# Kernel optimization log

Hardware: AMD Instinct MI355X
Metric: run time of the kernel (lower is better)

The kernel has to match this reference:

```python
import jax, jax.numpy as jnp
import numpy as np

B, S, D, H, L = 4, 2048, 256, 4, 2
DK = D // H
V, T = 32000, 1000


def setup_inputs() -> dict:
    key = jax.random.key(0)
    ks = jax.random.split(key, 20)
    sc = 0.02
    event_emb = jax.random.normal(ks[0], (V, D), jnp.float32) * sc
    event_emb = event_emb.at[0].set(0.0)  # padding_idx=0
    time_emb = jax.random.normal(ks[1], (T, D), jnp.float32) * sc
    inp = {
        "x": jax.random.randint(ks[2], (B, S), 0, V, jnp.int32),
        "time_deltas": jax.random.randint(ks[3], (B, S), 0, T, jnp.int32),
        "mask": jax.random.randint(ks[4], (B, S), 0, 2, jnp.int32),
        "event_emb": event_emb,
        "time_emb": time_emb,
        "Wq": jax.random.normal(ks[5], (L, D, D), jnp.float32) * sc,
        "bq": jnp.zeros((L, D), jnp.float32),
        "Wk": jax.random.normal(ks[6], (L, D, D), jnp.float32) * sc,
        "bk": jnp.zeros((L, D), jnp.float32),
        "Wv": jax.random.normal(ks[7], (L, D, D), jnp.float32) * sc,
        "bv": jnp.zeros((L, D), jnp.float32),
        "time_proj": jax.random.normal(ks[8], (L, T, H), jnp.float32) * sc,
        "Wo": jax.random.normal(ks[9], (L, D, D), jnp.float32) * sc,
        "bo": jnp.zeros((L, D), jnp.float32),
        "ln_g": jnp.ones((L, D), jnp.float32),
        "ln_b": jnp.zeros((L, D), jnp.float32),
        "Wc1": jax.random.normal(ks[10], (D, D // 2), jnp.float32) * sc,
        "bc1": jnp.zeros((D // 2,), jnp.float32),
        "Wc2": jax.random.normal(ks[11], (D // 2, 1), jnp.float32) * sc,
        "bc2": jnp.zeros((1,), jnp.float32),
    }
    return inp


def _layernorm(h, g, b, eps=1e-5):
    mu = jnp.mean(h, -1, keepdims=True)
    var = jnp.mean(jnp.square(h - mu), -1, keepdims=True)
    return (h - mu) * jax.lax.rsqrt(var + eps) * g + b


def _attn(h, t_bins, mask, Wq, bq, Wk, bk, Wv, bv, tp, Wo, bo):
    b, s, d = h.shape
    q = (h @ Wq + bq).reshape(b, s, H, DK)
    k = (h @ Wk + bk).reshape(b, s, H, DK)
    v = (h @ Wv + bv).reshape(b, s, H, DK)
    scores = jnp.einsum("bqhd,bkhd->bhqk", q, k) / np.sqrt(DK).astype(np.float32)
    time_bias = tp[t_bins]  # [b,s,H] -> bias per key position
    scores = scores + jnp.transpose(time_bias, (0, 2, 1))[:, :, None, :]
    scores = jnp.where(mask[:, None, None, :] == 0, -1e9, scores)
    attn = jax.nn.softmax(scores, axis=-1)
    ctx = jnp.einsum("bhqk,bkhd->bqhd", attn, v).reshape(b, s, d)
    return ctx @ Wo + bo


def reference(x, time_deltas, mask, event_emb, time_emb, Wq, bq, Wk, bk, Wv, bv,
              time_proj, Wo, bo, ln_g, ln_b, Wc1, bc1, Wc2, bc2):
    t_bins = jnp.clip(time_deltas, 0, T - 1)
    h = event_emb[x] + time_emb[t_bins]
    for l in range(L):
        h = _attn(h, t_bins, mask, Wq[l], bq[l], Wk[l], bk[l], Wv[l], bv[l],
                  time_proj[l], Wo[l], bo[l])
        h = _layernorm(h, ln_g[l], ln_b[l])
    last = h[:, -1, :]
    hid = jax.nn.relu(last @ Wc1 + bc1)
    return jax.nn.sigmoid(hid @ Wc2 + bc2)
```

## Files before the change

### kernel.cpp

```cpp
#include <hip/hip_runtime.h>
#include <math.h>

namespace {

constexpr int NB = 4, NS = 2048, ND = 256, NH = 4, NDK = 64, NL = 2, NT = 1000;
constexpr float L2E = 1.44269504089f;
constexpr float QSCALE = 0.125f * L2E;

typedef short bfx8 __attribute__((ext_vector_type(8)));
typedef float f32x4 __attribute__((ext_vector_type(4)));

static __device__ __forceinline__ short f2bf(float f) {
  union { float f; unsigned u; } v; v.f = f;
  unsigned u = v.u;
  unsigned r = (u + 0x7fffu + ((u >> 16) & 1u)) >> 16;
  return (short)r;
}
static __device__ __forceinline__ float exp2_hw(float x) {
  float r;
  asm("v_exp_f32 %0, %1" : "=v"(r) : "v"(x));
  return r;
}
static __device__ __forceinline__ unsigned cvt_pk_bf16(float lo, float hi) {
  unsigned d;
  asm("v_cvt_pk_bf16_f32 %0, %1, %2" : "=v"(d) : "v"(lo), "v"(hi));
  return d;
}

__global__ __launch_bounds__(256) void k_packw(const float* __restrict__ Wq,
                                               const float* __restrict__ Wk,
                                               const float* __restrict__ Wv,
                                               const float* __restrict__ Wo,
                                               short* __restrict__ wqkvT,
                                               short* __restrict__ woT) {
  __shared__ float t[64][65];
  int z = blockIdx.z, l = z >> 2, mat = z & 3;
  const float* src;
  short* dst;
  float scale = 1.f;
  if (mat == 0)      { src = Wq + (size_t)l * 65536; dst = wqkvT + (size_t)l * 768 * 256; scale = QSCALE; }
  else if (mat == 1) { src = Wk + (size_t)l * 65536; dst = wqkvT + (size_t)l * 768 * 256 + 256 * 256; }
  else if (mat == 2) { src = Wv + (size_t)l * 65536; dst = wqkvT + (size_t)l * 768 * 256 + 512 * 256; }
  else               { src = Wo + (size_t)l * 65536; dst = woT + (size_t)l * 65536; }
  int k0 = blockIdx.x * 64, n0 = blockIdx.y * 64;
  int c = threadIdx.x & 63, r4 = threadIdx.x >> 6;
  #pragma unroll
  for (int rr = 0; rr < 64; rr += 4) t[rr + r4][c] = src[(size_t)(k0 + rr + r4) * 256 + n0 + c];
  __syncthreads();
  #pragma unroll
  for (int rr = 0; rr < 64; rr += 4) {
    int n = rr + r4;
    dst[(size_t)(n0 + n) * 256 + k0 + c] = f2bf(t[c][n] * scale);
  }
}

__global__ __launch_bounds__(768) void k_packb(const float* __restrict__ bq,
                                               const float* __restrict__ bk,
                                               const float* __restrict__ bv,
                                               float* __restrict__ bqkv) {
  int l = blockIdx.x, c = threadIdx.x;
  float v;
  if (c < 256) v = bq[l * 256 + c] * QSCALE;
  else if (c < 512) v = bk[l * 256 + c - 256];
  else v = bv[l * 256 + c - 512];
  bqkv[l * 768 + c] = v;
}

__global__ __launch_bounds__(256) void k_embed(const int* __restrict__ x,
                                               const int* __restrict__ td,
                                               const float* __restrict__ ee,
                                               const float* __restrict__ te,
                                               float* __restrict__ h,
                                               short* __restrict__ hb) {
  int lane = threadIdx.x & 63, r4 = threadIdx.x >> 6;
  int row = blockIdx.x * 4 + r4;
  int xi = x[row];
  int tb = td[row];
  tb = tb < 0 ? 0 : (tb >= NT ? NT - 1 : tb);
  float4 e = ((const float4*)&ee[(size_t)xi * ND])[lane];
  float4 tv = ((const float4*)&te[(size_t)tb * ND])[lane];
  float4 v;
  v.x = e.x + tv.x; v.y = e.y + tv.y; v.z = e.z + tv.z; v.w = e.w + tv.w;
  ((float4*)&h[(size_t)row * ND])[lane] = v;
  short4 ob; ob.x = f2bf(v.x); ob.y = f2bf(v.y); ob.z = f2bf(v.z); ob.w = f2bf(v.w);
  ((short4*)&hb[(size_t)row * ND])[lane] = ob;
}

template <int OUT_BF16>
__global__ __launch_bounds__(256) void k_gemm(const short* __restrict__ A,
                                              const short* __restrict__ BT,
                                              const float* __restrict__ bias,
                                              void* __restrict__ C, int ldc,
                                              int mb_mul, int mb_add, int n_base) {
  constexpr int LP = 76;
  __shared__ short at[64][LP];
  __shared__ short bt[128][LP];
  int tid = threadIdx.x;
  int w = tid >> 6, lane = tid & 63, ln15 = lane & 15, g = lane >> 4;
  int m0 = (blockIdx.x * mb_mul + mb_add) * 64;
  int n0 = n_base + blockIdx.y * 128;
  int srow = tid >> 2, scol = (tid & 3) * 16;
  int brow = tid >> 1, bcol = (tid & 1) * 32;

  f32x4 acc[8];
  #pragma unroll
  for (int nt = 0; nt < 8; ++nt) acc[nt] = (f32x4){0.f, 0.f, 0.f, 0.f};

  bfx8 a0, a1, b0, b1, b2, b3;
  auto LOAD = [&](int kk0) {
    const short* as = &A[(size_t)(m0 + srow) * 256 + kk0 + scol];
    a0 = *(const bfx8*)as; a1 = *(const bfx8*)(as + 8);
    const short* bs = &BT[(size_t)(n0 + brow) * 256 + kk0 + bcol];
    b0 = *(const bfx8*)bs; b1 = *(const bfx8*)(bs + 8);
    b2 = *(const bfx8*)(bs + 16); b3 = *(const bfx8*)(bs + 24);
  };
  LOAD(0);
  for (int kk0 = 0; kk0 < 256; kk0 += 64) {
    __syncthreads();
    *(bfx8*)&at[srow][scol] = a0; *(bfx8*)&at[srow][scol + 8] = a1;
    *(bfx8*)&bt[brow][bcol] = b0; *(bfx8*)&bt[brow][bcol + 8] = b1;
    *(bfx8*)&bt[brow][bcol + 16] = b2; *(bfx8*)&bt[brow][bcol + 24] = b3;
    if (kk0 + 64 < 256) LOAD(kk0 + 64);
    __syncthreads();
    #pragma unroll
    for (int ks = 0; ks < 2; ++ks) {
      bfx8 af = *(const bfx8*)&at[w * 16 + ln15][ks * 32 + g * 8];
      #pragma unroll
      for (int nt = 0; nt < 8; ++nt) {
        bfx8 bf = *(const bfx8*)&bt[nt * 16 + ln15][ks * 32 + g * 8];
        acc[nt] = __builtin_amdgcn_mfma_f32_16x16x32_bf16(af, bf, acc[nt], 0, 0, 0);
      }
    }
  }

  #pragma unroll
  for (int nt = 0; nt < 8; ++nt) {
    int col = n0 + nt * 16 + ln15;
    float bb = bias[col];
    #pragma unroll
    for (int r = 0; r < 4; ++r) {
      int row = m0 + w * 16 + g * 4 + r;
      float val = acc[nt][r] + bb;
      if (OUT_BF16) ((short*)C)[(size_t)row * ldc + col] = f2bf(val);
      else          ((float*)C)[(size_t)row * ldc + col] = val;
    }
  }
}

__global__ __launch_bounds__(512, 4) void k_attn(const short* __restrict__ qkv,
                                                 const int* __restrict__ td,
                                                 const int* __restrict__ mask,
                                                 const float* __restrict__ tp,
                                                 short* __restrict__ ctx,
                                                 float* __restrict__ partO,
                                                 float* __restrict__ partML,
                                                 int q_base, int nchunk) {
  constexpr int LPK = 100;
  constexpr int LPV = 76;
  __shared__ short kt[2][64][LPK];
  __shared__ short vt[2][80][LPV];

  int tid = threadIdx.x;
  int w = tid >> 6, lane = tid & 63, ln15 = lane & 15, g = lane >> 4;
  int half = w >> 2, wsub = w & 3;
  int t = tid & 255;
  int b = blockIdx.z, hh = blockIdx.y;
  int qtile = blockIdx.x / nchunk;
  int chunk = blockIdx.x - qtile * nchunk;
  int niter = NS / (128 * nchunk);
  int kbase = chunk * (NS / nchunk);
  int q0 = q_base + qtile * 64;
  int qw0 = q0 + wsub * 16;

  for (int idx = tid; idx < 2 * 64 * 35; idx += 512) {
    int h2 = idx / (64 * 35), rem = idx % (64 * 35);
    kt[h2][rem / 35][65 + rem % 35] = 0;
  }
  for (int idx = tid; idx < 2 * 16 * LPV; idx += 512) {
    int h2 = idx / (16 * LPV), rem = idx % (16 * LPV), j = rem / LPV, c = rem % LPV;
    vt[h2][64 + j][c] = (j == 0 && c < 64) ? (short)0x3F80 : (short)0;
  }

  bfx8 aq[3];
  #pragma unroll
  for (int ks = 0; ks < 2; ++ks)
    aq[ks] = *(const bfx8*)&qkv[(size_t)(b * NS + qw0 + ln15) * 768 + hh * NDK + ks * 32 + g * 8];
  {
    bfx8 z = (bfx8){0, 0, 0, 0, 0, 0, 0, 0};
    if (g == 0) z[0] = (short)0x3F80;
    aq[2] = z;
  }

  f32x4 o[5];
  #pragma unroll
  for (int dt = 0; dt < 5; ++dt) o[dt] = (f32x4){0.f, 0.f, 0.f, 0.f};
  float m = -1e30f;

  int srow = t >> 2, scg = (t & 3) * 16;
  bool needB = (t & 3) == 0;
  int vlane = t & 63, vw4 = (t >> 6) & 3;
  int pks = vlane >> 5, ptt = (vlane >> 4) & 1, pgg = (vlane >> 2) & 3, prr = vlane & 3;
  int vcol = pks * 32 + pgg * 8 + ptt * 4 + prr;

  auto loadset = [&](int it, bfx8& KR0, bfx8& KR1, bfx8& VR0, bfx8& VR1, float& BR) {
    int k0 = kbase + (half * niter + it) * 64;
    const short* ksrc = &qkv[(size_t)(b * NS + k0 + srow) * 768 + 256 + hh * NDK + scg];
    KR0 = *(const bfx8*)ksrc; KR1 = *(const bfx8*)(ksrc + 8);
    const short* vsrc = &qkv[(size_t)(b * NS + k0 + vlane) * 768 + 512 + hh * NDK + vw4 * 16];
    VR0 = *(const bfx8*)vsrc; VR1 = *(const bfx8*)(vsrc + 8);
    if (needB) {
      int key = k0 + srow;
      int tb = td[b * NS + key];
      tb = tb < 0 ? 0 : (tb >= NT ? NT - 1 : tb);
      BR = mask[b * NS + key] ? tp[tb * NH + hh] * L2E : -1e9f;
    }
  };

  auto compute = [&]() {
    f32x4 c[4];
    #pragma unroll
    for (int nt = 0; nt < 4; ++nt) {
      c[nt] = (f32x4){0.f, 0.f, 0.f, 0.f};
      #pragma unroll
      for (int ks = 0; ks < 3; ++ks) {
        bfx8 kf = *(const bfx8*)&kt[half][nt * 16 + ln15][ks * 32 + g * 8];
        c[nt] = __builtin_amdgcn_mfma_f32_16x16x32_bf16(kf, aq[ks], c[nt], 0, 0, 0);
      }
    }
    float rm = c[0][0];
    #pragma unroll
    for (int nt = 0; nt < 4; ++nt)
      #pragma unroll
      for (int r = 0; r < 4; ++r) rm = fmaxf(rm, c[nt][r]);
    rm = fmaxf(rm, __shfl_xor(rm, 16, 64));
    rm = fmaxf(rm, __shfl_xor(rm, 32, 64));
    if (__any(rm > m + 10.f)) {
      float nm = fmaxf(m, rm);
      float scl = exp2_hw(m - nm);
      m = nm;
      #pragma unroll
      for (int dt = 0; dt < 5; ++dt)
        #pragma unroll
        for (int r = 0; r < 4; ++r) o[dt][r] *= scl;
    }
    unsigned pb[2][4];
    #pragma unroll
    for (int nt = 0; nt < 4; ++nt) {
      float e0 = exp2_hw(c[nt][0] - m), e1 = exp2_hw(c[nt][1] - m);
      float e2 = exp2_hw(c[nt][2] - m), e3 = exp2_hw(c[nt][3] - m);
      pb[nt >> 1][(nt & 1) * 2]     = cvt_pk_bf16(e0, e1);
      pb[nt >> 1][(nt & 1) * 2 + 1] = cvt_pk_bf16(e2, e3);
    }
    #pragma unroll
    for (int ks = 0; ks < 2; ++ks) {
      union { unsigned u[4]; bfx8 v; } pf;
      pf.u[0] = pb[ks][0]; pf.u[1] = pb[ks][1]; pf.u[2] = pb[ks][2]; pf.u[3] = pb[ks][3];
      #pragma unroll
      for (int dt = 0; dt < 5; ++dt) {
        bfx8 vf = *(const bfx8*)&vt[half][dt * 16 + ln15][ks * 32 + g * 8];
        o[dt] = __builtin_amdgcn_mfma_f32_16x16x32_bf16(vf, pf.v, o[dt], 0, 0, 0);
      }
    }
  };

  auto body = [&](bfx8& KR0, bfx8& KR1, bfx8& VR0, bfx8& VR1, float& BR,
                  int pf_it, bool do_pf) {
    __syncthreads();
    *(bfx8*)&kt[half][srow][scg] = KR0;
    *(bfx8*)&kt[half][srow][scg + 8] = KR1;
    if (needB) kt[half][srow][64] = f2bf(BR);
    #pragma unroll
    for (int i = 0; i < 8; ++i) {
      vt[half][vw4 * 16 + i][vcol] = VR0[i];
      vt[half][vw4 * 16 + 8 + i][vcol] = VR1[i];
    }
    if (do_pf) loadset(pf_it, KR0, KR1, VR0, VR1, BR);
    __syncthreads();
    compute();
  };

  bfx8 krA0, krA1, vrA0, vrA1; float brA = 0.f;
  bfx8 krB0, krB1, vrB0, vrB1; float brB = 0.f;
  loadset(0, krA0, krA1, vrA0, vrA1, brA);
  if (niter > 1) loadset(1, krB0, krB1, vrB0, vrB1, brB);

  for (int it = 0; it < niter; it += 2) {
    body(krA0, krA1, vrA0, vrA1, brA, it + 2, it + 2 < niter);
    if (it + 1 < niter)
      body(krB0, krB1, vrB0, vrB1, brB, it + 3, it + 3 < niter);
  }

  float* shO = (float*)&kt[0][0][0];
  float* shML = (float*)&vt[0][0][0];
  __syncthreads();
  int q = wsub * 16 + ln15;
  if (half == 1) {
    #pragma unroll
    for (int dt = 0; dt < 4; ++dt) {
      float4 st; st.x = o[dt][0]; st.y = o[dt][1]; st.z = o[dt][2]; st.w = o[dt][3];
      *(float4*)&shO[q * 68 + dt * 16 + g * 4] = st;
    }
    if (g == 0) { shML[q * 2] = m; shML[q * 2 + 1] = o[4][0]; }
  }
  __syncthreads();
  if (half == 0) {
    float l = __shfl(o[4][0], ln15, 64);
    float m2 = shML[q * 2], l2 = shML[q * 2 + 1];
    float M = fmaxf(m, m2);
    float fa = exp2_hw(m - M), fb = exp2_hw(m2 - M);
    if (nchunk == 1) {
      float inv = 1.f / (l * fa + l2 * fb);
      fa *= inv; fb *= inv;
      #pragma unroll
      for (int dt = 0; dt < 4; ++dt) {
        float4 sh = *(const float4*)&shO[q * 68 + dt * 16 + g * 4];
        float v0 = o[dt][0] * fa + sh.x * fb;
        float v1 = o[dt][1] * fa + sh.y * fb;
        float v2 = o[dt][2] * fa + sh.z * fb;
        float v3 = o[dt][3] * fa + sh.w * fb;
        int2 pk; pk.x = (int)cvt_pk_bf16(v0, v1); pk.y = (int)cvt_pk_bf16(v2, v3);
        *(int2*)&ctx[(size_t)(b * NS + q0 + q) * ND + hh * NDK + dt * 16 + g * 4] = pk;
      }
    } else {
      float L = l * fa + l2 * fb;
      size_t pidx = (size_t)(chunk * NB + b) * NH + hh;
      #pragma unroll
      for (int dt = 0; dt < 4; ++dt) {
        float4 sh = *(const float4*)&shO[q * 68 + dt * 16 + g * 4];
        float4 st;
        st.x = o[dt][0] * fa + sh.x * fb;
        st.y = o[dt][1] * fa + sh.y * fb;
        st.z = o[dt][2] * fa + sh.z * fb;
        st.w = o[dt][3] * fa + sh.w * fb;
        *(float4*)&partO[pidx * 4096 + q * 64 + dt * 16 + g * 4] = st;
      }
      if (g == 0) { partML[pidx * 128 + q * 2] = M; partML[pidx * 128 + q * 2 + 1] = L; }
    }
  }
}

__global__ __launch_bounds__(256) void k_amerge(const float* __restrict__ partO,
                                                const float* __restrict__ partML,
                                                short* __restrict__ ctx,
                                                int q_base, int nchunk) {
  int b = blockIdx.x, hh = blockIdx.y;
  int q = threadIdx.x >> 2, d0 = (threadIdx.x & 3) * 16;
  float M = -1e30f;
  for (int c = 0; c < nchunk; ++c)
    M = fmaxf(M, partML[((size_t)(c * NB + b) * NH + hh) * 128 + q * 2]);
  float L = 0.f;
  float acc[16];
  #pragma unroll
  for (int i = 0; i < 16; ++i) acc[i] = 0.f;
  for (int c = 0; c < nchunk; ++c) {
    size_t pidx = (size_t)(c * NB + b) * NH + hh;
    float mc = partML[pidx * 128 + q * 2];
    float lc = partML[pidx * 128 + q * 2 + 1];
    float s = exp2_hw(mc - M);
    L += lc * s;
    const float4* op = (const float4*)&partO[pidx * 4096 + q * 64 + d0];
    #pragma unroll
    for (int i = 0; i < 4; ++i) {
      float4 v = op[i];
      acc[i * 4]     += v.x * s;
      acc[i * 4 + 1] += v.y * s;
      acc[i * 4 + 2] += v.z * s;
      acc[i * 4 + 3] += v.w * s;
    }
  }
  float inv = 1.f / L;
  short res[16];
  #pragma unroll
  for (int i = 0; i < 16; ++i) res[i] = f2bf(acc[i] * inv);
  int4 pk = *(const int4*)res;
  *(int4*)&ctx[(size_t)(b * NS + q_base + q) * ND + hh * NDK + d0] = pk;
}

__global__ __launch_bounds__(256) void k_ln(float* __restrict__ h,
                                            short* __restrict__ hb,
                                            const float* __restrict__ g_,
                                            const float* __restrict__ b_, int q_base) {
  int lane = threadIdx.x & 63, r4 = threadIdx.x >> 6;
  size_t row = (size_t)blockIdx.y * NS + q_base + blockIdx.x * 4 + r4;
  float4 v = ((const float4*)&h[row * ND])[lane];
  float s = v.x + v.y + v.z + v.w;
  #pragma unroll
  for (int off = 1; off < 64; off <<= 1) s += __shfl_xor(s, off, 64);
  float mu = s * (1.f / ND);
  float dx = v.x - mu, dy = v.y - mu, dz = v.z - mu, dw = v.w - mu;
  float q = dx * dx + dy * dy + dz * dz + dw * dw;
  #pragma unroll
  for (int off = 1; off < 64; off <<= 1) q += __shfl_xor(q, off, 64);
  float rr = rsqrtf(q * (1.f / ND) + 1e-5f);
  float4 gg = ((const float4*)g_)[lane];
  float4 bb = ((const float4*)b_)[lane];
  float4 o;
  o.x = dx * rr * gg.x + bb.x;
  o.y = dy * rr * gg.y + bb.y;
  o.z = dz * rr * gg.z + bb.z;
  o.w = dw * rr * gg.w + bb.w;
  ((float4*)&h[row * ND])[lane] = o;
  short4 ob; ob.x = f2bf(o.x); ob.y = f2bf(o.y); ob.z = f2bf(o.z); ob.w = f2bf(o.w);
  ((short4*)&hb[row * ND])[lane] = ob;
}

__global__ __launch_bounds__(128) void k_head(const float* __restrict__ h,
                                              const float* __restrict__ Wc1,
                                              const float* __restrict__ bc1,
                                              const float* __restrict__ Wc2,
                                              const float* __restrict__ bc2,
                                              float* __restrict__ out) {
  __shared__ float red[128];
  int j = threadIdx.x;
  int b = blockIdx.x;
  const float* last = &h[(size_t)(b * NS + NS - 1) * ND];
  float acc = bc1[j];
  for (int d = 0; d < ND; ++d) acc = fmaf(last[d], Wc1[d * 128 + j], acc);
  acc = fmaxf(acc, 0.f);
  red[j] = acc * Wc2[j];
  __syncthreads();
  for (int off = 64; off > 0; off >>= 1) {
    if (j < off) red[j] += red[j + off];
    __syncthreads();
  }
  if (j == 0) out[b] = 1.f / (1.f + __expf(-(red[0] + bc2[0])));
}

}

extern "C" void kernel_launch(void* const* d_in, const int* in_sizes, int n_in,
                              void* d_out, int out_size, void* d_ws, size_t ws_size,
                              hipStream_t stream) {
  const int* x = (const int*)d_in[0];
  const int* td = (const int*)d_in[1];
  const int* mask = (const int*)d_in[2];
  const float* ee = (const float*)d_in[3];
  const float* te = (const float*)d_in[4];
  const float* Wq = (const float*)d_in[5];
  const float* bq = (const float*)d_in[6];
  const float* Wk = (const float*)d_in[7];
  const float* bk = (const float*)d_in[8];
  const float* Wv = (const float*)d_in[9];
  const float* bv = (const float*)d_in[10];
  const float* tp = (const float*)d_in[11];
  const float* Wo = (const float*)d_in[12];
  const float* bo = (const float*)d_in[13];
  const float* lng = (const float*)d_in[14];
  const float* lnb = (const float*)d_in[15];
  const float* Wc1 = (const float*)d_in[16];
  const float* bc1 = (const float*)d_in[17];
  const float* Wc2 = (const float*)d_in[18];
  const float* bc2 = (const float*)d_in[19];
  float* out = (float*)d_out;

  char* ws = (char*)d_ws;
  const size_t M = (size_t)NB * NS;
  float* h      = (float*)(ws);
  short* hb     = (short*)(ws + (8 << 20));
  short* qkv    = (short*)(ws + (12 << 20));
  short* ctx    = (short*)(ws + (24 << 20));
  short* wqkvT  = (short*)(ws + (28 << 20));
  short* woT    = (short*)(ws + (28 << 20) + 786432);
  float* bqkv   = (float*)(ws + (29 << 20) + 262144);
  float* partO  = (float*)(ws + (30 << 20));
  float* partML = (float*)(ws + (34 << 20) + (256 << 10));

  k_packw<<<dim3(4, 4, 8), 256, 0, stream>>>(Wq, Wk, Wv, Wo, wqkvT, woT);
  k_packb<<<2, 768, 0, stream>>>(bq, bk, bv, bqkv);
  k_embed<<<NB * NS / 4, 256, 0, stream>>>(x, td, ee, te, h, hb);

  for (int l = 0; l < NL; ++l) {
    const short* wqkvTl = wqkvT + (size_t)l * 768 * 256;
    const short* woTl = woT + (size_t)l * 65536;
    const float* bqkvl = bqkv + (size_t)l * 768;
    const float* bol = bo + (size_t)l * ND;
    const float* tpl = tp + (size_t)l * NT * NH;
    const float* lngl = lng + (size_t)l * ND;
    const float* lnbl = lnb + (size_t)l * ND;
    const bool last = (l == NL - 1);

    if (!last) {
      k_gemm<1><<<dim3(M / 64, 6), 256, 0, stream>>>(hb, wqkvTl, bqkvl, qkv, 768, 1, 0, 0);
    } else {
      k_gemm<1><<<dim3(M / 64, 4), 256, 0, stream>>>(hb, wqkvTl, bqkvl, qkv, 768, 1, 0, 256);
      k_gemm<1><<<dim3(NB, 2), 256, 0, stream>>>(hb, wqkvTl, bqkvl, qkv, 768, 32, 31, 0);
    }

    if (!last) {
      k_attn<<<dim3(NS / 64, NH, NB), 512, 0, stream>>>(qkv, td, mask, tpl, ctx,
                                                        nullptr, nullptr, 0, 1);
      k_gemm<0><<<dim3(M / 64, 2), 256, 0, stream>>>(ctx, woTl, bol, h, 256, 1, 0, 0);
      k_ln<<<dim3(NS / 4, NB), 256, 0, stream>>>(h, hb, lngl, lnbl, 0);
    } else {
      k_attn<<<dim3(16, NH, NB), 512, 0, stream>>>(qkv, td, mask, tpl, ctx,
                                                   partO, partML, NS - 64, 16);
      k_amerge<<<dim3(NB, NH), 256, 0, stream>>>(partO, partML, ctx, NS - 64, 16);
      k_gemm<0><<<dim3(NB, 2), 256, 0, stream>>>(ctx, woTl, bol, h, 256, 32, 31, 0);
      k_ln<<<dim3(1, NB), 256, 0, stream>>>(h, hb, lngl, lnbl, NS - 4);
    }
  }

  k_head<<<NB, 128, 0, stream>>>(h, Wc1, bc1, Wc2, bc2, out);
}
```

Measured before the change: 139.9 us.

## Split first-layer attention over two key chunks with bf16 partials and merge kernel

The first layer's attention now splits each query tile's key range into two chunks, doubling the block count. The chunks write bf16 partial outputs and their max/sum statistics, and a k_amerge pass then combines them. The partial buffers are moved into the workspace at offset 0, and the bias packing is folded into k_packw, removing one launch. s_setprio hints are added around the MFMA sections. The extra kernel launch and the bf16 round-trip of partial outputs cost time and lower precision in exchange for more parallelism. The partO buffer now overlaps h, which is only safe if h is not live during attention.

```diff
diff --git a/kernel.cpp b/kernel.cpp
--- a/kernel.cpp
+++ b/kernel.cpp
@@ -16,6 +16,10 @@
   unsigned r = (u + 0x7fffu + ((u >> 16) & 1u)) >> 16;
   return (short)r;
 }
+static __device__ __forceinline__ float bf2f(short s) {
+  union { float f; unsigned u; } v; v.u = ((unsigned)(unsigned short)s) << 16;
+  return v.f;
+}
 static __device__ __forceinline__ float exp2_hw(float x) {
   float r;
   asm("v_exp_f32 %0, %1" : "=v"(r) : "v"(x));
@@ -31,8 +35,12 @@
                                                const float* __restrict__ Wk,
                                                const float* __restrict__ Wv,
                                                const float* __restrict__ Wo,
+                                               const float* __restrict__ bq,
+                                               const float* __restrict__ bk,
+                                               const float* __restrict__ bv,
                                                short* __restrict__ wqkvT,
-                                               short* __restrict__ woT) {
+                                               short* __restrict__ woT,
+                                               float* __restrict__ bqkv) {
   __shared__ float t[64][65];
   int z = blockIdx.z, l = z >> 2, mat = z & 3;
   const float* src;
@@ -52,18 +60,13 @@
     int n = rr + r4;
     dst[(size_t)(n0 + n) * 256 + k0 + c] = f2bf(t[c][n] * scale);
   }
-}
-
-__global__ __launch_bounds__(768) void k_packb(const float* __restrict__ bq,
-                                               const float* __restrict__ bk,
-                                               const float* __restrict__ bv,
-                                               float* __restrict__ bqkv) {
-  int l = blockIdx.x, c = threadIdx.x;
-  float v;
-  if (c < 256) v = bq[l * 256 + c] * QSCALE;
-  else if (c < 512) v = bk[l * 256 + c - 256];
-  else v = bv[l * 256 + c - 512];
-  bqkv[l * 768 + c] = v;
+  if (mat == 0 && blockIdx.x == 0 && blockIdx.y == 0) {
+    for (int cc = threadIdx.x; cc < 768; cc += 256) {
+      float v = cc < 256 ? bq[l * 256 + cc] * QSCALE
+                         : (cc < 512 ? bk[l * 256 + cc - 256] : bv[l * 256 + cc - 512]);
+      bqkv[l * 768 + cc] = v;
+    }
+  }
 }
 
 __global__ __launch_bounds__(256) void k_embed(const int* __restrict__ x,
@@ -152,9 +155,9 @@
                                                  const int* __restrict__ mask,
                                                  const float* __restrict__ tp,
                                                  short* __restrict__ ctx,
-                                                 float* __restrict__ partO,
+                                                 short* __restrict__ partO,
                                                  float* __restrict__ partML,
-                                                 int q_base, int nchunk) {
+                                                 int q_base, int qcount, int nchunk) {
   constexpr int LPK = 100;
   constexpr int LPV = 76;
   __shared__ short kt[2][64][LPK];
@@ -218,6 +221,7 @@
 
   auto compute = [&]() {
     f32x4 c[4];
+    __builtin_amdgcn_s_setprio(1);
     #pragma unroll
     for (int nt = 0; nt < 4; ++nt) {
       c[nt] = (f32x4){0.f, 0.f, 0.f, 0.f};
@@ -227,6 +231,7 @@
         c[nt] = __builtin_amdgcn_mfma_f32_16x16x32_bf16(kf, aq[ks], c[nt], 0, 0, 0);
       }
     }
+    __builtin_amdgcn_s_setprio(0);
     float rm = c[0][0];
     #pragma unroll
     for (int nt = 0; nt < 4; ++nt)
@@ -251,6 +256,7 @@
       pb[nt >> 1][(nt & 1) * 2]     = cvt_pk_bf16(e0, e1);
       pb[nt >> 1][(nt & 1) * 2 + 1] = cvt_pk_bf16(e2, e3);
     }
+    __builtin_amdgcn_s_setprio(1);
     #pragma unroll
     for (int ks = 0; ks < 2; ++ks) {
       union { unsigned u[4]; bfx8 v; } pf;
@@ -261,6 +267,7 @@
         o[dt] = __builtin_amdgcn_mfma_f32_16x16x32_bf16(vf, pf.v, o[dt], 0, 0, 0);
       }
     }
+    __builtin_amdgcn_s_setprio(0);
   };
 
   auto body = [&](bfx8& KR0, bfx8& KR1, bfx8& VR0, bfx8& VR1, float& BR,
@@ -323,57 +330,59 @@
       }
     } else {
       float L = l * fa + l2 * fb;
-      size_t pidx = (size_t)(chunk * NB + b) * NH + hh;
+      size_t rowi = (size_t)(chunk * 16 + b * NH + hh) * qcount + qtile * 64 + q;
       #pragma unroll
       for (int dt = 0; dt < 4; ++dt) {
         float4 sh = *(const float4*)&shO[q * 68 + dt * 16 + g * 4];
-        float4 st;
-        st.x = o[dt][0] * fa + sh.x * fb;
-        st.y = o[dt][1] * fa + sh.y * fb;
-        st.z = o[dt][2] * fa + sh.z * fb;
-        st.w = o[dt][3] * fa + sh.w * fb;
-        *(float4*)&partO[pidx * 4096 + q * 64 + dt * 16 + g * 4] = st;
+        float v0 = o[dt][0] * fa + sh.x * fb;
+        float v1 = o[dt][1] * fa + sh.y * fb;
+        float v2 = o[dt][2] * fa + sh.z * fb;
+        float v3 = o[dt][3] * fa + sh.w * fb;
+        int2 pk; pk.x = (int)cvt_pk_bf16(v0, v1); pk.y = (int)cvt_pk_bf16(v2, v3);
+        *(int2*)&partO[rowi * 64 + dt * 16 + g * 4] = pk;
       }
-      if (g == 0) { partML[pidx * 128 + q * 2] = M; partML[pidx * 128 + q * 2 + 1] = L; }
-    }
-  }
-}
-
-__global__ __launch_bounds__(256) void k_amerge(const float* __restrict__ partO,
+      if (g == 0) { partML[rowi * 2] = M; partML[rowi * 2 + 1] = L; }
+    }
+  }
+}
+
+__global__ __launch_bounds__(256) void k_amerge(const short* __restrict__ partO,
                                                 const float* __restrict__ partML,
                                                 short* __restrict__ ctx,
-                                                int q_base, int nchunk) {
-  int b = blockIdx.x, hh = blockIdx.y;
-  int q = threadIdx.x >> 2, d0 = (threadIdx.x & 3) * 16;
+                                                int q_base, int qcount, int nchunk) {
+  int b = blockIdx.z, hh = blockIdx.y;
+  int qi = blockIdx.x * 64 + (threadIdx.x >> 2);
+  int d0 = (threadIdx.x & 3) * 16;
+  int bh = b * NH + hh;
   float M = -1e30f;
   for (int c = 0; c < nchunk; ++c)
-    M = fmaxf(M, partML[((size_t)(c * NB + b) * NH + hh) * 128 + q * 2]);
+    M = fmaxf(M, partML[((size_t)(c * 16 + bh) * qcount + qi) * 2]);
   float L = 0.f;
   float acc[16];
   #pragma unroll
   for (int i = 0; i < 16; ++i) acc[i] = 0.f;
   for (int c = 0; c < nchunk; ++c) {
-    size_t pidx = (size_t)(c * NB + b) * NH + hh;
-    float mc = partML[pidx * 128 + q * 2];
-    float lc = partML[pidx * 128 + q * 2 + 1];
+    size_t row = (size_t)(c * 16 + bh) * qcount + qi;
+    float mc = partML[row * 2];
+    float lc = partML[row * 2 + 1];
     float s = exp2_hw(mc - M);
     L += lc * s;
-    const float4* op = (const float4*)&partO[pidx * 4096 + q * 64 + d0];
-    #pragma unroll
-    for (int i = 0; i < 4; ++i) {
-      float4 v = op[i];
-      acc[i * 4]     += v.x * s;
-      acc[i * 4 + 1] += v.y * s;
-      acc[i * 4 + 2] += v.z * s;
-      acc[i * 4 + 3] += v.w * s;
+    union { int4 v; short sh[8]; } u0, u1;
+    u0.v = *(const int4*)&partO[row * 64 + d0];
+    u1.v = *(const int4*)&partO[row * 64 + d0 + 8];
+    #pragma unroll
+    for (int i = 0; i < 8; ++i) {
+      acc[i]     += bf2f(u0.sh[i]) * s;
+      acc[8 + i] += bf2f(u1.sh[i]) * s;
     }
   }
   float inv = 1.f / L;
   short res[16];
   #pragma unroll
   for (int i = 0; i < 16; ++i) res[i] = f2bf(acc[i] * inv);
-  int4 pk = *(const int4*)res;
-  *(int4*)&ctx[(size_t)(b * NS + q_base + q) * ND + hh * NDK + d0] = pk;
+  short* dst = &ctx[(size_t)(b * NS + q_base + qi) * ND + hh * NDK + d0];
+  *(int4*)dst = *(const int4*)res;
+  *(int4*)(dst + 8) = *(const int4*)(res + 8);
 }
 
 __global__ __launch_bounds__(256) void k_ln(float* __restrict__ h,
@@ -462,11 +471,10 @@
   short* wqkvT  = (short*)(ws + (28 << 20));
   short* woT    = (short*)(ws + (28 << 20) + 786432);
   float* bqkv   = (float*)(ws + (29 << 20) + 262144);
-  float* partO  = (float*)(ws + (30 << 20));
-  float* partML = (float*)(ws + (34 << 20) + (256 << 10));
-
-  k_packw<<<dim3(4, 4, 8), 256, 0, stream>>>(Wq, Wk, Wv, Wo, wqkvT, woT);
-  k_packb<<<2, 768, 0, stream>>>(bq, bk, bv, bqkv);
+  short* partO  = (short*)(ws);
+  float* partML = (float*)(ws + (10 << 20));
+
+  k_packw<<<dim3(4, 4, 8), 256, 0, stream>>>(Wq, Wk, Wv, Wo, bq, bk, bv, wqkvT, woT, bqkv);
   k_embed<<<NB * NS / 4, 256, 0, stream>>>(x, td, ee, te, h, hb);
 
   for (int l = 0; l < NL; ++l) {
@@ -487,14 +495,15 @@
     }
 
     if (!last) {
-      k_attn<<<dim3(NS / 64, NH, NB), 512, 0, stream>>>(qkv, td, mask, tpl, ctx,
-                                                        nullptr, nullptr, 0, 1);
+      k_attn<<<dim3((NS / 64) * 2, NH, NB), 512, 0, stream>>>(qkv, td, mask, tpl, ctx,
+                                                              partO, partML, 0, NS, 2);
+      k_amerge<<<dim3(NS / 64, NH, NB), 256, 0, stream>>>(partO, partML, ctx, 0, NS, 2);
       k_gemm<0><<<dim3(M / 64, 2), 256, 0, stream>>>(ctx, woTl, bol, h, 256, 1, 0, 0);
       k_ln<<<dim3(NS / 4, NB), 256, 0, stream>>>(h, hb, lngl, lnbl, 0);
     } else {
       k_attn<<<dim3(16, NH, NB), 512, 0, stream>>>(qkv, td, mask, tpl, ctx,
-                                                   partO, partML, NS - 64, 16);
-      k_amerge<<<dim3(NB, NH), 256, 0, stream>>>(partO, partML, ctx, NS - 64, 16);
+                                                   partO, partML, NS - 64, 64, 16);
+      k_amerge<<<dim3(1, NH, NB), 256, 0, stream>>>(partO, partML, ctx, NS - 64, 64, 16);
       k_gemm<0><<<dim3(NB, 2), 256, 0, stream>>>(ctx, woTl, bol, h, 256, 32, 31, 0);
       k_ln<<<dim3(1, NB), 256, 0, stream>>>(h, hb, lngl, lnbl, NS - 4);
     }
```

New measurement: 150.5 us. 1.08x slower.
